# Kernel tuning notes

Hardware: AMD Instinct MI355X
Metric: run time of the kernel (lower is better)

The kernel has to match this reference:

```python
import jax, jax.numpy as jnp
import numpy as np

D, H, DK, DFF = 256, 8, 32, 1024
EPS = 1e-5

def _layernorm(x, g, b):
    mu = jnp.mean(x, axis=-1, keepdims=True)
    var = jnp.mean((x - mu) ** 2, axis=-1, keepdims=True)
    return (x - mu) * jax.lax.rsqrt(var + EPS) * g + b

def setup_inputs() -> dict:
    key = jax.random.key(0)
    ks = jax.random.split(key, 16)
    s = 1.0 / np.sqrt(D)
    sf = 1.0 / np.sqrt(DFF)
    return {
        "src": jax.random.normal(ks[0], (2, 4096, D), jnp.float32),
        "Wq": jax.random.uniform(ks[1], (H, D, DK), jnp.float32, -s, s),
        "bq": jax.random.uniform(ks[2], (H, DK), jnp.float32, -s, s),
        "Wk": jax.random.uniform(ks[3], (H, D, DK), jnp.float32, -s, s),
        "bk": jax.random.uniform(ks[4], (H, DK), jnp.float32, -s, s),
        "Wv": jax.random.uniform(ks[5], (H, D, DK), jnp.float32, -s, s),
        "bv": jax.random.uniform(ks[6], (H, DK), jnp.float32, -s, s),
        "Wo": jax.random.uniform(ks[7], (H * DK, D), jnp.float32, -s, s),
        "bo": jax.random.uniform(ks[8], (D,), jnp.float32, -s, s),
        "ln1_g": jnp.ones((D,), jnp.float32),
        "ln1_b": jnp.zeros((D,), jnp.float32),
        "W1": jax.random.uniform(ks[9], (D, DFF), jnp.float32, -s, s),
        "b1": jax.random.uniform(ks[10], (DFF,), jnp.float32, -s, s),
        "W2": jax.random.uniform(ks[11], (DFF, D), jnp.float32, -sf, sf),
        "b2": jax.random.uniform(ks[12], (D,), jnp.float32, -sf, sf),
        "ln2_g": jnp.ones((D,), jnp.float32),
        "ln2_b": jnp.zeros((D,), jnp.float32),
    }

def reference(src, Wq, bq, Wk, bk, Wv, bv, Wo, bo, ln1_g, ln1_b, W1, b1, W2, b2, ln2_g, ln2_b):
    B, S, _ = src.shape
    # per-head projections, batched over heads: [B,H,S,DK]
    q = jnp.einsum("bsd,hdk->bhsk", src, Wq) + bq[None, :, None, :]
    k = jnp.einsum("bsd,hdk->bhsk", src, Wk) + bk[None, :, None, :]
    v = jnp.einsum("bsd,hdk->bhsk", src, Wv) + bv[None, :, None, :]
    scale = jnp.sqrt(jnp.asarray(DK, src.dtype))
    scores = jnp.einsum("bhsk,bhtk->bhst", q, k) / scale  # [B,H,S,S]
    attn = jax.nn.softmax(scores, axis=-1)
    ctx = jnp.einsum("bhst,bhtv->bhsv", attn, v)  # [B,H,S,DK]
    ctx = ctx.transpose(0, 2, 1, 3).reshape(B, S, H * DK)  # concat heads
    attn_out = ctx @ Wo + bo
    x = _layernorm(src + attn_out, ln1_g, ln1_b)  # post-LN residual (dropout=0)
    ffn = jnp.maximum(x @ W1 + b1, 0.0) @ W2 + b2
    return _layernorm(x + ffn, ln2_g, ln2_b)
```

## Files before the change

### kernel.cpp

```cpp
#include <hip/hip_runtime.h>
#include <hip/hip_bf16.h>

#define BB   2
#define SS   4096
#define DD   256
#define HH   8
#define DKK  32
#define DFFC 1024
#define BS   (BB*SS)
#define MB   (1024*1024)

#define SCALE2 (0.17677669529663689f * 1.4426950408889634f)

typedef float f32x4 __attribute__((ext_vector_type(4)));
typedef __bf16 bf16x8 __attribute__((ext_vector_type(8)));

static __device__ __forceinline__ unsigned int cvtpk2(float lo, float hi) {
    unsigned int r;
    asm("v_cvt_pk_bf16_f32 %0, %1, %2" : "=v"(r) : "v"(lo), "v"(hi));
    return r;
}
static __device__ __forceinline__ unsigned short f2bf(float f) {
    return (unsigned short)cvtpk2(f, 0.0f);
}

__global__ __launch_bounds__(256) void convert_k(
    const float* __restrict__ src,
    const float* __restrict__ Wq, const float* __restrict__ Wk,
    const float* __restrict__ Wv, const float* __restrict__ Wo,
    const float* __restrict__ W1, const float* __restrict__ W2,
    const float* __restrict__ bq, const float* __restrict__ bk,
    const float* __restrict__ bv,
    unsigned short* __restrict__ srcb, unsigned short* __restrict__ Wqkv_t,
    unsigned short* __restrict__ Wo_t, unsigned short* __restrict__ W1_t,
    unsigned short* __restrict__ W2_t, float* __restrict__ bqkv)
{
    int idx = blockIdx.x * 256 + threadIdx.x;
    if (idx < 2097152) { srcb[idx] = f2bf(src[idx]); return; }
    int i = idx - 2097152;
    if (i < 196608) {
        const int c = i >> 8, d = i & 255;
        const int which = c >> 8, h = (c >> 5) & 7, kk = c & 31;
        const float* W = which == 0 ? Wq : which == 1 ? Wk : Wv;
        Wqkv_t[i] = f2bf(W[h * 8192 + d * 32 + kk]);
        return;
    }
    i -= 196608;
    if (i < 65536) {
        const int n = i >> 8, k2 = i & 255;
        Wo_t[i] = f2bf(Wo[k2 * 256 + n]);
        return;
    }
    i -= 65536;
    if (i < 262144) {
        const int n = i >> 8, k2 = i & 255;
        W1_t[i] = f2bf(W1[k2 * 1024 + n]);
        return;
    }
    i -= 262144;
    if (i < 262144) {
        const int n = i >> 10, k2 = i & 1023;
        W2_t[i] = f2bf(W2[k2 * 256 + n]);
        return;
    }
    i -= 262144;
    if (i < 768)
        bqkv[i] = (i < 256) ? bq[i] : (i < 512) ? bk[i - 256] : bv[i - 512];
}

#define LDA 36

template <int EPI, int K, int BM>
__global__ __launch_bounds__(256) void mfma_gemm_k(
    const unsigned short* __restrict__ A,
    const unsigned short* __restrict__ Bt,
    const float* __restrict__ bias,
    const float* __restrict__ Rres,
    void* __restrict__ Cout, int N)
{
    constexpr int MI = BM / 32;
    __shared__ unsigned short Al[BM * LDA];
    __shared__ unsigned short Bl[64 * LDA];

    const int tid  = threadIdx.x;
    const int w    = tid >> 6, lane = tid & 63;
    const int lq   = lane & 15, lk = lane >> 4;
    const int wr   = w >> 1,   wc = w & 1;
    const int m0   = blockIdx.y * BM, n0 = blockIdx.x * 64;

    const int arow = (BM == 128) ? (tid >> 1) : (tid >> 2);
    const int ac   = (BM == 128) ? ((tid & 1) * 16) : ((tid & 3) * 8);
    const int brow = tid >> 2, bc = (tid & 3) * 8;
    const unsigned short* Ap = A  + (size_t)(m0 + arow) * K + ac;
    const unsigned short* Bp = Bt + (size_t)(n0 + brow) * K + bc;

    f32x4 acc[MI][2];
#pragma unroll
    for (int mi = 0; mi < MI; ++mi)
#pragma unroll
        for (int ni = 0; ni < 2; ++ni) acc[mi][ni] = (f32x4){0.f, 0.f, 0.f, 0.f};

    int4 a0, a1, b0;
    a0 = *(const int4*)(Ap);
    if constexpr (BM == 128) a1 = *(const int4*)(Ap + 8);
    b0 = *(const int4*)(Bp);

    for (int k0 = 0; k0 < K; k0 += 32) {
        __syncthreads();
        *(int4*)&Al[arow * LDA + ac] = a0;
        if constexpr (BM == 128) *(int4*)&Al[arow * LDA + ac + 8] = a1;
        *(int4*)&Bl[brow * LDA + bc] = b0;
        __syncthreads();
        if (k0 + 32 < K) {
            a0 = *(const int4*)(Ap + k0 + 32);
            if constexpr (BM == 128) a1 = *(const int4*)(Ap + k0 + 40);
            b0 = *(const int4*)(Bp + k0 + 32);
        }

        bf16x8 bfrag[2];
#pragma unroll
        for (int ni = 0; ni < 2; ++ni)
            bfrag[ni] = *(const bf16x8*)&Bl[(wc * 32 + ni * 16 + lq) * LDA + lk * 8];
#pragma unroll
        for (int mi = 0; mi < MI; ++mi) {
            const bf16x8 afrag =
                *(const bf16x8*)&Al[(wr * (BM / 2) + mi * 16 + lq) * LDA + lk * 8];
#pragma unroll
            for (int ni = 0; ni < 2; ++ni)
                acc[mi][ni] = __builtin_amdgcn_mfma_f32_16x16x32_bf16(
                    afrag, bfrag[ni], acc[mi][ni], 0, 0, 0);
        }
    }

#pragma unroll
    for (int ni = 0; ni < 2; ++ni) {
        const int col = n0 + wc * 32 + ni * 16 + lq;
        const float bv_ = bias[col];
#pragma unroll
        for (int mi = 0; mi < MI; ++mi) {
#pragma unroll
            for (int r = 0; r < 4; ++r) {
                const int row = m0 + wr * (BM / 2) + mi * 16 + lk * 4 + r;
                float val = acc[mi][ni][r] + bv_;
                if constexpr (EPI == 0) {
                    ((float*)Cout)[(size_t)row * N + col] =
                        val + Rres[(size_t)row * N + col];
                } else if constexpr (EPI == 1) {
                    ((unsigned short*)Cout)[(size_t)row * N + col] =
                        f2bf(fmaxf(val, 0.f));
                } else {
                    const int which = col >> 8, h = (col >> 5) & 7, kk = col & 31;
                    if (which == 0) val *= SCALE2;
                    const int b = row >> 12, s = row & (SS - 1);
                    ((unsigned short*)Cout)[(size_t)which * 2097152 +
                        ((size_t)(b * 8 + h) * SS + s) * 32 + kk] = f2bf(val);
                }
            }
        }
    }
}

#define KVB 128
#define RK  40
#define RVT 136
#define RVP 136

__global__ __launch_bounds__(256) void attn_mfma_k(
    const unsigned short* __restrict__ qb, const unsigned short* __restrict__ kb,
    const unsigned short* __restrict__ vb, unsigned short* __restrict__ ctxb)
{
    __shared__ unsigned short Kl[KVB * RK];
    __shared__ unsigned short Vt[32 * RVT];
    __shared__ unsigned short Pl[4][16 * RVP];

    const int tid  = threadIdx.x;
    const int w    = tid >> 6;
    const int lane = tid & 63;
    const int lq   = lane & 15;
    const int lk   = lane >> 4;
    const int bh   = blockIdx.x;
    const int b    = bh >> 3;
    const int h    = bh & 7;
    const int q0   = blockIdx.y * 64;

    const int rho  = tid >> 1, ksel = tid & 1;
    const int kgt  = ((rho & 15) << 3) | (rho >> 4);
    const int vt   = tid & 127, vh = (tid >> 7) * 16;

    const unsigned short* kg = kb + (size_t)bh * SS * DKK;
    const unsigned short* vg = vb + (size_t)bh * SS * DKK;

    union U16 { int4 i; bf16x8 b; unsigned short s[8]; };

    U16 uq;
    uq.i = *(const int4*)(qb + ((size_t)bh * SS + q0 + w * 16 + lq) * DKK + lk * 8);
    const bf16x8 aq = uq.b;

    float m_[4], l_[4];
    f32x4 o0 = {0.f, 0.f, 0.f, 0.f};
    f32x4 o1 = {0.f, 0.f, 0.f, 0.f};
#pragma unroll
    for (int r = 0; r < 4; ++r) { m_[r] = -INFINITY; l_[r] = 0.f; }

    int4 ka0 = *(const int4*)(kg + (size_t)kgt * DKK + ksel * 16);
    int4 ka1 = *(const int4*)(kg + (size_t)kgt * DKK + ksel * 16 + 8);
    int4 va0 = *(const int4*)(vg + (size_t)vt * DKK + vh);
    int4 va1 = *(const int4*)(vg + (size_t)vt * DKK + vh + 8);

    for (int t0 = 0; t0 < SS; t0 += KVB) {
        __syncthreads();
        *(int4*)&Kl[rho * RK + ksel * 16]     = ka0;
        *(int4*)&Kl[rho * RK + ksel * 16 + 8] = ka1;
        U16 u0, u1; u0.i = va0; u1.i = va1;
#pragma unroll
        for (int j = 0; j < 8; ++j) {
            Vt[(vh + j) * RVT + vt]     = u0.s[j];
            Vt[(vh + 8 + j) * RVT + vt] = u1.s[j];
        }
        __syncthreads();

        if (t0 + KVB < SS) {
            const unsigned short* kn = kg + (size_t)(t0 + KVB) * DKK;
            const unsigned short* vn = vg + (size_t)(t0 + KVB) * DKK;
            ka0 = *(const int4*)(kn + (size_t)kgt * DKK + ksel * 16);
            ka1 = *(const int4*)(kn + (size_t)kgt * DKK + ksel * 16 + 8);
            va0 = *(const int4*)(vn + (size_t)vt * DKK + vh);
            va1 = *(const int4*)(vn + (size_t)vt * DKK + vh + 8);
        }

        f32x4 acc[8];
#pragma unroll
        for (int g = 0; g < 8; ++g) {
            const bf16x8 bk_ = *(const bf16x8*)&Kl[(g * 16 + lq) * RK + lk * 8];
            acc[g] = __builtin_amdgcn_mfma_f32_16x16x32_bf16(
                aq, bk_, (f32x4){0.f, 0.f, 0.f, 0.f}, 0, 0, 0);
        }

        float rm[4];
#pragma unroll
        for (int r = 0; r < 4; ++r) {
            float v = acc[0][r];
#pragma unroll
            for (int g = 1; g < 8; ++g) v = fmaxf(v, acc[g][r]);
            v = fmaxf(v, __shfl_xor(v, 1));
            v = fmaxf(v, __shfl_xor(v, 2));
            v = fmaxf(v, __shfl_xor(v, 4));
            v = fmaxf(v, __shfl_xor(v, 8));
            rm[r] = v;
        }
        const bool grow = (rm[0] > m_[0] + 8.f) || (rm[1] > m_[1] + 8.f) ||
                          (rm[2] > m_[2] + 8.f) || (rm[3] > m_[3] + 8.f);
        if (__any(grow)) {
#pragma unroll
            for (int r = 0; r < 4; ++r) {
                const float mn = fmaxf(m_[r], rm[r]);
                const float c  = exp2f(m_[r] - mn);
                m_[r] = mn;
                l_[r] *= c;
                o0[r] *= c;
                o1[r] *= c;
            }
        }
#pragma unroll
        for (int r = 0; r < 4; ++r) {
            float p[8];
            float s = 0.f;
#pragma unroll
            for (int g = 0; g < 8; ++g) {
                p[g] = exp2f(acc[g][r] - m_[r]);
                s += p[g];
            }
            l_[r] += s;
            int4 pi;
            pi.x = (int)cvtpk2(p[0], p[1]);
            pi.y = (int)cvtpk2(p[2], p[3]);
            pi.z = (int)cvtpk2(p[4], p[5]);
            pi.w = (int)cvtpk2(p[6], p[7]);
            *(int4*)&Pl[w][(lk * 4 + r) * RVP + lq * 8] = pi;
        }

#pragma unroll
        for (int c2 = 0; c2 < 4; ++c2) {
            const bf16x8 pa = *(const bf16x8*)&Pl[w][lq * RVP + c2 * 32 + lk * 8];
            const bf16x8 v0 = *(const bf16x8*)&Vt[lq * RVT + c2 * 32 + lk * 8];
            o0 = __builtin_amdgcn_mfma_f32_16x16x32_bf16(pa, v0, o0, 0, 0, 0);
            const bf16x8 v1 = *(const bf16x8*)&Vt[(16 + lq) * RVT + c2 * 32 + lk * 8];
            o1 = __builtin_amdgcn_mfma_f32_16x16x32_bf16(pa, v1, o1, 0, 0, 0);
        }
    }

#pragma unroll
    for (int r = 0; r < 4; ++r) {
        float ls = l_[r];
        ls += __shfl_xor(ls, 1);
        ls += __shfl_xor(ls, 2);
        ls += __shfl_xor(ls, 4);
        ls += __shfl_xor(ls, 8);
        const float inv = 1.0f / ls;
        const size_t row = (size_t)b * SS + q0 + w * 16 + lk * 4 + r;
        unsigned short* cp = ctxb + row * (HH * DKK) + h * DKK;
        cp[lq]      = f2bf(o0[r] * inv);
        cp[16 + lq] = f2bf(o1[r] * inv);
    }
}

__global__ __launch_bounds__(256) void ln_k(
    const float* __restrict__ y, const float* __restrict__ g,
    const float* __restrict__ be, float* __restrict__ out,
    unsigned short* __restrict__ outb)
{
    const int tid = threadIdx.x;
    const size_t r = blockIdx.x;
    const float val = y[r * DD + tid];
    float s1 = val, s2 = val * val;
#pragma unroll
    for (int i = 1; i < 64; i <<= 1) {
        s1 += __shfl_xor(s1, i, 64);
        s2 += __shfl_xor(s2, i, 64);
    }
    __shared__ float ps1[4], ps2[4];
    const int w = tid >> 6, lane = tid & 63;
    if (lane == 0) { ps1[w] = s1; ps2[w] = s2; }
    __syncthreads();
    const float t1 = ps1[0] + ps1[1] + ps1[2] + ps1[3];
    const float t2 = ps2[0] + ps2[1] + ps2[2] + ps2[3];
    const float mean = t1 * (1.f / DD);
    const float var  = t2 * (1.f / DD) - mean * mean;
    const float rs   = rsqrtf(var + 1e-5f);
    const float res  = (val - mean) * rs * g[tid] + be[tid];
    out[r * DD + tid] = res;
    if (outb) outb[r * DD + tid] = f2bf(res);
}

extern "C" void kernel_launch(void* const* d_in, const int* in_sizes, int n_in,
                              void* d_out, int out_size, void* d_ws, size_t ws_size,
                              hipStream_t stream)
{
    const float* src  = (const float*)d_in[0];
    const float* Wq   = (const float*)d_in[1];
    const float* bq   = (const float*)d_in[2];
    const float* Wk   = (const float*)d_in[3];
    const float* bk   = (const float*)d_in[4];
    const float* Wv   = (const float*)d_in[5];
    const float* bv   = (const float*)d_in[6];
    const float* Wo   = (const float*)d_in[7];
    const float* bo   = (const float*)d_in[8];
    const float* ln1g = (const float*)d_in[9];
    const float* ln1b = (const float*)d_in[10];
    const float* W1   = (const float*)d_in[11];
    const float* b1   = (const float*)d_in[12];
    const float* W2   = (const float*)d_in[13];
    const float* b2   = (const float*)d_in[14];
    const float* ln2g = (const float*)d_in[15];
    const float* ln2b = (const float*)d_in[16];
    float* out = (float*)d_out;

    char* wsb = (char*)d_ws;
    float*          x     = (float*)(wsb);
    unsigned short* xb    = (unsigned short*)(wsb + (size_t) 8 * MB);
    unsigned short* srcb  = (unsigned short*)(wsb + (size_t)12 * MB);
    unsigned short* qb    = (unsigned short*)(wsb + (size_t)16 * MB);
    unsigned short* kb2   = (unsigned short*)(wsb + (size_t)20 * MB);
    unsigned short* vb2   = (unsigned short*)(wsb + (size_t)24 * MB);
    unsigned short* ctxb  = (unsigned short*)(wsb + (size_t)28 * MB);
    float*          y1    = (float*)(wsb + (size_t)32 * MB);
    unsigned short* hh    = (unsigned short*)(wsb + (size_t)12 * MB);
    unsigned short* Wqkv_t= (unsigned short*)(wsb + (size_t)40 * MB);
    unsigned short* Wo_t  = (unsigned short*)(wsb + (size_t)40 * MB + 384 * 1024);
    unsigned short* W1_t  = (unsigned short*)(wsb + (size_t)40 * MB + 512 * 1024);
    unsigned short* W2_t  = (unsigned short*)(wsb + (size_t)40 * MB + 1024 * 1024);
    float*          bqkv  = (float*)(wsb + (size_t)40 * MB + 1536 * 1024);

    convert_k<<<11267, 256, 0, stream>>>(src, Wq, Wk, Wv, Wo, W1, W2, bq, bk, bv,
                                         srcb, Wqkv_t, Wo_t, W1_t, W2_t, bqkv);

    mfma_gemm_k<2, DD, 128><<<dim3(12, 64), 256, 0, stream>>>(
        srcb, Wqkv_t, bqkv, nullptr, qb, 768);

    attn_mfma_k<<<dim3(BB * HH, SS / 64), 256, 0, stream>>>(qb, kb2, vb2, ctxb);

    mfma_gemm_k<0, DD, 64><<<dim3(4, 128), 256, 0, stream>>>(
        ctxb, Wo_t, bo, src, y1, DD);

    ln_k<<<BS, DD, 0, stream>>>(y1, ln1g, ln1b, x, xb);

    mfma_gemm_k<1, DD, 128><<<dim3(16, 64), 256, 0, stream>>>(
        xb, W1_t, b1, nullptr, hh, DFFC);

    mfma_gemm_k<0, DFFC, 64><<<dim3(4, 128), 256, 0, stream>>>(
        hh, W2_t, b2, x, out, DD);

    ln_k<<<BS, DD, 0, stream>>>(out, ln2g, ln2b, out, nullptr);
}
```

Before: 284.6 us.

## Load K/V fragments directly from global via permuted K and pre-transposed V

The attention kernel no longer stages K and V tiles in shared memory with block-wide barriers. The QKV GEMM epilogue writes K in a permuted row order, and a new kernel transposes V, so each wave can load its MFMA operands straight from global/L2 in 64-key steps. The row-sum is now computed by an MFMA against a ones vector instead of shuffles, and the max shuffles run only when the rescale branch triggers. This trades the LDS traffic and barriers for more global/L2 traffic per wave, since each of the four waves reloads K/V independently, plus one extra transpose launch. The workspace buffers are also remapped.

```diff
diff --git a/kernel.cpp b/kernel.cpp
--- a/kernel.cpp
+++ b/kernel.cpp
@@ -47,20 +47,17 @@
     }
     i -= 196608;
     if (i < 65536) {
-        const int n = i >> 8, k2 = i & 255;
-        Wo_t[i] = f2bf(Wo[k2 * 256 + n]);
+        Wo_t[i] = f2bf(Wo[(i & 255) * 256 + (i >> 8)]);
         return;
     }
     i -= 65536;
     if (i < 262144) {
-        const int n = i >> 8, k2 = i & 255;
-        W1_t[i] = f2bf(W1[k2 * 1024 + n]);
+        W1_t[i] = f2bf(W1[(i & 255) * 1024 + (i >> 8)]);
         return;
     }
     i -= 262144;
     if (i < 262144) {
-        const int n = i >> 10, k2 = i & 1023;
-        W2_t[i] = f2bf(W2[k2 * 256 + n]);
+        W2_t[i] = f2bf(W2[(i & 1023) * 256 + (i >> 10)]);
         return;
     }
     i -= 262144;
@@ -151,7 +148,10 @@
                 } else {
                     const int which = col >> 8, h = (col >> 5) & 7, kk = col & 31;
                     if (which == 0) val *= SCALE2;
-                    const int b = row >> 12, s = row & (SS - 1);
+                    const int b = row >> 12;
+                    int s = row & (SS - 1);
+                    if (which == 1)
+                        s = (s & ~63) | (((s & 3) << 4) | ((s & 63) >> 2));
                     ((unsigned short*)Cout)[(size_t)which * 2097152 +
                         ((size_t)(b * 8 + h) * SS + s) * 32 + kk] = f2bf(val);
                 }
@@ -160,18 +160,28 @@
     }
 }
 
-#define KVB 128
-#define RK  40
-#define RVT 136
-#define RVP 136
+__global__ __launch_bounds__(256) void vT_k(
+    const unsigned short* __restrict__ vb, unsigned short* __restrict__ vbT)
+{
+    const int tid = threadIdx.x;
+    const int bh  = blockIdx.x >> 6;
+    const int s0  = (blockIdx.x & 63) * 64;
+    const int kk  = tid >> 3;
+    const int sp  = (tid & 7) * 8;
+    const unsigned short* src = vb + ((size_t)bh * SS + s0 + sp) * DKK + kk;
+    union { int4 i; unsigned short s[8]; } u;
+#pragma unroll
+    for (int j = 0; j < 8; ++j) u.s[j] = src[(size_t)j * DKK];
+    *(int4*)(vbT + ((size_t)bh * DKK + kk) * SS + s0 + sp) = u.i;
+}
+
+#define RP 72
 
 __global__ __launch_bounds__(256) void attn_mfma_k(
-    const unsigned short* __restrict__ qb, const unsigned short* __restrict__ kb,
-    const unsigned short* __restrict__ vb, unsigned short* __restrict__ ctxb)
-{
-    __shared__ unsigned short Kl[KVB * RK];
-    __shared__ unsigned short Vt[32 * RVT];
-    __shared__ unsigned short Pl[4][16 * RVP];
+    const unsigned short* __restrict__ qb, const unsigned short* __restrict__ kbP,
+    const unsigned short* __restrict__ vbT, unsigned short* __restrict__ ctxb)
+{
+    __shared__ unsigned short Pl[4][16 * RP];
 
     const int tid  = threadIdx.x;
     const int w    = tid >> 6;
@@ -183,120 +193,91 @@
     const int h    = bh & 7;
     const int q0   = blockIdx.y * 64;
 
-    const int rho  = tid >> 1, ksel = tid & 1;
-    const int kgt  = ((rho & 15) << 3) | (rho >> 4);
-    const int vt   = tid & 127, vh = (tid >> 7) * 16;
-
-    const unsigned short* kg = kb + (size_t)bh * SS * DKK;
-    const unsigned short* vg = vb + (size_t)bh * SS * DKK;
-
-    union U16 { int4 i; bf16x8 b; unsigned short s[8]; };
+    union U16 { int4 i; bf16x8 v; };
 
     U16 uq;
     uq.i = *(const int4*)(qb + ((size_t)bh * SS + q0 + w * 16 + lq) * DKK + lk * 8);
-    const bf16x8 aq = uq.b;
-
-    float m_[4], l_[4];
-    f32x4 o0 = {0.f, 0.f, 0.f, 0.f};
-    f32x4 o1 = {0.f, 0.f, 0.f, 0.f};
-#pragma unroll
-    for (int r = 0; r < 4; ++r) { m_[r] = -INFINITY; l_[r] = 0.f; }
-
-    int4 ka0 = *(const int4*)(kg + (size_t)kgt * DKK + ksel * 16);
-    int4 ka1 = *(const int4*)(kg + (size_t)kgt * DKK + ksel * 16 + 8);
-    int4 va0 = *(const int4*)(vg + (size_t)vt * DKK + vh);
-    int4 va1 = *(const int4*)(vg + (size_t)vt * DKK + vh + 8);
-
-    for (int t0 = 0; t0 < SS; t0 += KVB) {
-        __syncthreads();
-        *(int4*)&Kl[rho * RK + ksel * 16]     = ka0;
-        *(int4*)&Kl[rho * RK + ksel * 16 + 8] = ka1;
-        U16 u0, u1; u0.i = va0; u1.i = va1;
-#pragma unroll
-        for (int j = 0; j < 8; ++j) {
-            Vt[(vh + j) * RVT + vt]     = u0.s[j];
-            Vt[(vh + 8 + j) * RVT + vt] = u1.s[j];
-        }
-        __syncthreads();
-
-        if (t0 + KVB < SS) {
-            const unsigned short* kn = kg + (size_t)(t0 + KVB) * DKK;
-            const unsigned short* vn = vg + (size_t)(t0 + KVB) * DKK;
-            ka0 = *(const int4*)(kn + (size_t)kgt * DKK + ksel * 16);
-            ka1 = *(const int4*)(kn + (size_t)kgt * DKK + ksel * 16 + 8);
-            va0 = *(const int4*)(vn + (size_t)vt * DKK + vh);
-            va1 = *(const int4*)(vn + (size_t)vt * DKK + vh + 8);
-        }
-
-        f32x4 acc[8];
-#pragma unroll
-        for (int g = 0; g < 8; ++g) {
-            const bf16x8 bk_ = *(const bf16x8*)&Kl[(g * 16 + lq) * RK + lk * 8];
+    const bf16x8 aq = uq.v;
+
+    const unsigned short* kl0 = kbP + (size_t)bh * SS * DKK + (size_t)lq * DKK + lk * 8;
+    const unsigned short* vl0 = vbT + (size_t)bh * DKK * SS + (size_t)lq * SS + lk * 8;
+
+    const int4 onesi = make_int4(0x3F803F80, 0x3F803F80, 0x3F803F80, 0x3F803F80);
+    U16 uo; uo.i = onesi;
+    const bf16x8 onesb = uo.v;
+
+    float m_[4];
+    f32x4 o0   = {0.f, 0.f, 0.f, 0.f};
+    f32x4 o1   = {0.f, 0.f, 0.f, 0.f};
+    f32x4 lacc = {0.f, 0.f, 0.f, 0.f};
+#pragma unroll
+    for (int r = 0; r < 4; ++r) m_[r] = -INFINITY;
+
+    for (int t0 = 0; t0 < SS; t0 += 64) {
+        U16 kf[4], vf[4];
+#pragma unroll
+        for (int g = 0; g < 4; ++g)
+            kf[g].i = *(const int4*)(kl0 + (size_t)(t0 + g * 16) * DKK);
+#pragma unroll
+        for (int c2 = 0; c2 < 2; ++c2) {
+            vf[c2 * 2 + 0].i = *(const int4*)(vl0 + t0 + c2 * 32);
+            vf[c2 * 2 + 1].i = *(const int4*)(vl0 + (size_t)16 * SS + t0 + c2 * 32);
+        }
+
+        f32x4 acc[4];
+#pragma unroll
+        for (int g = 0; g < 4; ++g)
             acc[g] = __builtin_amdgcn_mfma_f32_16x16x32_bf16(
-                aq, bk_, (f32x4){0.f, 0.f, 0.f, 0.f}, 0, 0, 0);
-        }
-
-        float rm[4];
-#pragma unroll
-        for (int r = 0; r < 4; ++r) {
-            float v = acc[0][r];
-#pragma unroll
-            for (int g = 1; g < 8; ++g) v = fmaxf(v, acc[g][r]);
-            v = fmaxf(v, __shfl_xor(v, 1));
-            v = fmaxf(v, __shfl_xor(v, 2));
-            v = fmaxf(v, __shfl_xor(v, 4));
-            v = fmaxf(v, __shfl_xor(v, 8));
-            rm[r] = v;
-        }
-        const bool grow = (rm[0] > m_[0] + 8.f) || (rm[1] > m_[1] + 8.f) ||
-                          (rm[2] > m_[2] + 8.f) || (rm[3] > m_[3] + 8.f);
+                aq, kf[g].v, (f32x4){0.f, 0.f, 0.f, 0.f}, 0, 0, 0);
+
+        float rml[4];
+#pragma unroll
+        for (int r = 0; r < 4; ++r)
+            rml[r] = fmaxf(fmaxf(acc[0][r], acc[1][r]),
+                           fmaxf(acc[2][r], acc[3][r]));
+        const bool grow = (rml[0] > m_[0] + 8.f) || (rml[1] > m_[1] + 8.f) ||
+                          (rml[2] > m_[2] + 8.f) || (rml[3] > m_[3] + 8.f);
         if (__any(grow)) {
 #pragma unroll
             for (int r = 0; r < 4; ++r) {
-                const float mn = fmaxf(m_[r], rm[r]);
+                float v = rml[r];
+                v = fmaxf(v, __shfl_xor(v, 1));
+                v = fmaxf(v, __shfl_xor(v, 2));
+                v = fmaxf(v, __shfl_xor(v, 4));
+                v = fmaxf(v, __shfl_xor(v, 8));
+                const float mn = fmaxf(m_[r], v);
                 const float c  = exp2f(m_[r] - mn);
                 m_[r] = mn;
-                l_[r] *= c;
+                lacc[r] *= c;
                 o0[r] *= c;
                 o1[r] *= c;
             }
         }
+
 #pragma unroll
         for (int r = 0; r < 4; ++r) {
-            float p[8];
-            float s = 0.f;
-#pragma unroll
-            for (int g = 0; g < 8; ++g) {
-                p[g] = exp2f(acc[g][r] - m_[r]);
-                s += p[g];
-            }
-            l_[r] += s;
-            int4 pi;
-            pi.x = (int)cvtpk2(p[0], p[1]);
-            pi.y = (int)cvtpk2(p[2], p[3]);
-            pi.z = (int)cvtpk2(p[4], p[5]);
-            pi.w = (int)cvtpk2(p[6], p[7]);
-            *(int4*)&Pl[w][(lk * 4 + r) * RVP + lq * 8] = pi;
-        }
-
-#pragma unroll
-        for (int c2 = 0; c2 < 4; ++c2) {
-            const bf16x8 pa = *(const bf16x8*)&Pl[w][lq * RVP + c2 * 32 + lk * 8];
-            const bf16x8 v0 = *(const bf16x8*)&Vt[lq * RVT + c2 * 32 + lk * 8];
-            o0 = __builtin_amdgcn_mfma_f32_16x16x32_bf16(pa, v0, o0, 0, 0, 0);
-            const bf16x8 v1 = *(const bf16x8*)&Vt[(16 + lq) * RVT + c2 * 32 + lk * 8];
-            o1 = __builtin_amdgcn_mfma_f32_16x16x32_bf16(pa, v1, o1, 0, 0, 0);
+            const float p0 = exp2f(acc[0][r] - m_[r]);
+            const float p1 = exp2f(acc[1][r] - m_[r]);
+            const float p2 = exp2f(acc[2][r] - m_[r]);
+            const float p3 = exp2f(acc[3][r] - m_[r]);
+            int2 pw;
+            pw.x = (int)cvtpk2(p0, p1);
+            pw.y = (int)cvtpk2(p2, p3);
+            *(int2*)&Pl[w][(lk * 4 + r) * RP + lq * 4] = pw;
+        }
+
+#pragma unroll
+        for (int c2 = 0; c2 < 2; ++c2) {
+            const bf16x8 pa = *(const bf16x8*)&Pl[w][lq * RP + c2 * 32 + lk * 8];
+            lacc = __builtin_amdgcn_mfma_f32_16x16x32_bf16(pa, onesb, lacc, 0, 0, 0);
+            o0 = __builtin_amdgcn_mfma_f32_16x16x32_bf16(pa, vf[c2*2+0].v, o0, 0, 0, 0);
+            o1 = __builtin_amdgcn_mfma_f32_16x16x32_bf16(pa, vf[c2*2+1].v, o1, 0, 0, 0);
         }
     }
 
 #pragma unroll
     for (int r = 0; r < 4; ++r) {
-        float ls = l_[r];
-        ls += __shfl_xor(ls, 1);
-        ls += __shfl_xor(ls, 2);
-        ls += __shfl_xor(ls, 4);
-        ls += __shfl_xor(ls, 8);
-        const float inv = 1.0f / ls;
+        const float inv = 1.0f / lacc[r];
         const size_t row = (size_t)b * SS + q0 + w * 16 + lk * 4 + r;
         unsigned short* cp = ctxb + row * (HH * DKK) + h * DKK;
         cp[lq]      = f2bf(o0[r] * inv);
@@ -360,16 +341,17 @@
     unsigned short* xb    = (unsigned short*)(wsb + (size_t) 8 * MB);
     unsigned short* srcb  = (unsigned short*)(wsb + (size_t)12 * MB);
     unsigned short* qb    = (unsigned short*)(wsb + (size_t)16 * MB);
-    unsigned short* kb2   = (unsigned short*)(wsb + (size_t)20 * MB);
+    unsigned short* kbP   = (unsigned short*)(wsb + (size_t)20 * MB);
     unsigned short* vb2   = (unsigned short*)(wsb + (size_t)24 * MB);
-    unsigned short* ctxb  = (unsigned short*)(wsb + (size_t)28 * MB);
-    float*          y1    = (float*)(wsb + (size_t)32 * MB);
-    unsigned short* hh    = (unsigned short*)(wsb + (size_t)12 * MB);
-    unsigned short* Wqkv_t= (unsigned short*)(wsb + (size_t)40 * MB);
-    unsigned short* Wo_t  = (unsigned short*)(wsb + (size_t)40 * MB + 384 * 1024);
-    unsigned short* W1_t  = (unsigned short*)(wsb + (size_t)40 * MB + 512 * 1024);
-    unsigned short* W2_t  = (unsigned short*)(wsb + (size_t)40 * MB + 1024 * 1024);
-    float*          bqkv  = (float*)(wsb + (size_t)40 * MB + 1536 * 1024);
+    unsigned short* vbT   = (unsigned short*)(wsb + (size_t)28 * MB);
+    unsigned short* ctxb  = (unsigned short*)(wsb + (size_t)32 * MB);
+    float*          y1    = (float*)(wsb + (size_t)16 * MB);
+    unsigned short* hh    = (unsigned short*)(wsb + (size_t)20 * MB);
+    unsigned short* Wqkv_t= (unsigned short*)(wsb + (size_t)36 * MB);
+    unsigned short* Wo_t  = (unsigned short*)(wsb + (size_t)36 * MB + 384 * 1024);
+    unsigned short* W1_t  = (unsigned short*)(wsb + (size_t)36 * MB + 512 * 1024);
+    unsigned short* W2_t  = (unsigned short*)(wsb + (size_t)36 * MB + 1024 * 1024);
+    float*          bqkv  = (float*)(wsb + (size_t)36 * MB + 1536 * 1024);
 
     convert_k<<<11267, 256, 0, stream>>>(src, Wq, Wk, Wv, Wo, W1, W2, bq, bk, bv,
                                          srcb, Wqkv_t, Wo_t, W1_t, W2_t, bqkv);
@@ -377,7 +359,9 @@
     mfma_gemm_k<2, DD, 128><<<dim3(12, 64), 256, 0, stream>>>(
         srcb, Wqkv_t, bqkv, nullptr, qb, 768);
 
-    attn_mfma_k<<<dim3(BB * HH, SS / 64), 256, 0, stream>>>(qb, kb2, vb2, ctxb);
+    vT_k<<<1024, 256, 0, stream>>>(vb2, vbT);
+
+    attn_mfma_k<<<dim3(BB * HH, SS / 64), 256, 0, stream>>>(qb, kbP, vbT, ctxb);
 
     mfma_gemm_k<0, DD, 64><<<dim3(4, 128), 256, 0, stream>>>(
         ctxb, Wo_t, bo, src, y1, DD);
```

New measurement: 333.8 us. 17.3% more time.
